# Performance work log

Hardware: AMD Instinct MI355X
Metric: run time of the kernel (lower is better)

Reference implementation:

```python
import jax, jax.numpy as jnp
import numpy as np

EMBED_DIM = 1024
VALUE_DIM = 2048
NUM_HEADS = 8
KEY_DIM = EMBED_DIM // NUM_HEADS      # 128
HEAD_DIM = VALUE_DIM // NUM_HEADS     # 256
B, T = 2, 2048
EPS = 1e-6


def _rotate_every_two(x):
    # x: [..., d] with d even; pairs (x0,x1)->(-x1,x0)
    x1 = x[..., ::2]
    x2 = x[..., 1::2]
    return jnp.stack((-x2, x1), axis=-1).reshape(x.shape)


def _theta_shift(x, sin, cos):
    # sin/cos: [T, key_dim] broadcast over [B, H, T, key_dim]
    return x * cos + _rotate_every_two(x) * sin


def setup_inputs() -> dict:
    key = jax.random.key(0)
    ks = jax.random.split(key, 6)
    x = jax.random.normal(ks[0], (B, T, EMBED_DIM), dtype=jnp.float32)

    # rotary angles as in torchscale RetNetRelPos
    angle = 1.0 / (10000.0 ** jnp.linspace(0.0, 1.0, KEY_DIM // 2))
    angle = jnp.repeat(angle, 2)                       # [key_dim], interleaved pairs
    idx = jnp.arange(T, dtype=jnp.float32)
    sin = jnp.sin(idx[:, None] * angle[None, :])       # [T, key_dim]
    cos = jnp.cos(idx[:, None] * angle[None, :])

    # per-head decay mask, normalized by sqrt(row-sum) as in RetNet
    decay = jnp.log(1.0 - 2.0 ** (-5.0 - jnp.arange(NUM_HEADS, dtype=jnp.float32)))
    diff = idx[:, None] - idx[None, :]                 # [T, T]
    exponent = jnp.where(diff >= 0, decay[:, None, None] * diff[None], -jnp.inf)
    mask = jnp.exp(exponent)                           # [H, T, T], lower-triangular decay
    mask = mask / jnp.sqrt(mask.sum(-1, keepdims=True))

    s = 0.02
    Wq = s * jax.random.normal(ks[1], (EMBED_DIM, EMBED_DIM), dtype=jnp.float32)
    Wk = s * jax.random.normal(ks[2], (EMBED_DIM, EMBED_DIM), dtype=jnp.float32)
    Wv = s * jax.random.normal(ks[3], (EMBED_DIM, VALUE_DIM), dtype=jnp.float32)
    Wg = s * jax.random.normal(ks[4], (EMBED_DIM, VALUE_DIM), dtype=jnp.float32)
    Wo = s * jax.random.normal(ks[5], (VALUE_DIM, EMBED_DIM), dtype=jnp.float32)
    return {"x": x, "sin": sin, "cos": cos, "mask": mask,
            "Wq": Wq, "Wk": Wk, "Wv": Wv, "Wg": Wg, "Wo": Wo}


def reference(x, sin, cos, mask, Wq, Wk, Wv, Wg, Wo):
    bsz, tgt_len, _ = x.shape
    scaling = KEY_DIM ** (-0.5)

    q = x @ Wq
    k = (x @ Wk) * scaling
    v = x @ Wv
    g = x @ Wg

    q = q.reshape(bsz, tgt_len, NUM_HEADS, KEY_DIM).transpose(0, 2, 1, 3)  # [B,H,T,kd]
    k = k.reshape(bsz, tgt_len, NUM_HEADS, KEY_DIM).transpose(0, 2, 1, 3)
    qr = _theta_shift(q, sin, cos)
    kr = _theta_shift(k, sin, cos)

    vr = v.reshape(bsz, tgt_len, NUM_HEADS, HEAD_DIM).transpose(0, 2, 1, 3)  # [B,H,T,hd]

    # parallel retention: decay-masked QK^T with abs-sum normalization (detached)
    qk = jnp.einsum('bhtd,bhsd->bhts', qr, kr) * mask[None]
    denom = jnp.clip(jnp.sum(jnp.abs(jax.lax.stop_gradient(qk)), axis=-1, keepdims=True),
                     1.0, 50000.0)
    qk = qk / denom
    out = jnp.einsum('bhts,bhsd->bhtd', qk, vr)          # [B,H,T,hd]
    out = out.transpose(0, 2, 1, 3)                      # [B,T,H,hd]

    # per-head RMSNorm (no affine)
    out = out * jax.lax.rsqrt(jnp.mean(out * out, axis=-1, keepdims=True) + EPS)
    out = out.reshape(bsz, tgt_len, VALUE_DIM)

    out = jax.nn.silu(g) * out
    return out @ Wo
```

## Files before the change

kernel.cpp:

```cpp
#include <hip/hip_runtime.h>
#include <hip/hip_bf16.h>
#include <math.h>

constexpr int T_SEQ = 2048;
constexpr int BB    = 2;
constexpr int EMBED = 1024;
constexpr int VDIM  = 2048;
constexpr int NHEADS = 8;
constexpr int KDIM  = 128;
constexpr int HDIM  = 256;
constexpr int ROWS  = BB * T_SEQ;
constexpr float EPS = 1e-6f;

typedef float  f32x4  __attribute__((ext_vector_type(4)));
typedef __bf16 bf16x8 __attribute__((ext_vector_type(8)));
typedef __bf16 bf16x4 __attribute__((ext_vector_type(4)));

__device__ __forceinline__ void gload16(const void* g, void* l) {
    __builtin_amdgcn_global_load_lds(
        (__attribute__((address_space(1))) void*)g,
        (__attribute__((address_space(3))) void*)l, 16, 0, 0);
}

#define WAITV(n) asm volatile("s_waitcnt vmcnt(" #n ")" ::: "memory")
#define BARRIER() __builtin_amdgcn_s_barrier()

__global__ __launch_bounds__(256)
void prep_all(const float* __restrict__ x, const float* __restrict__ Wq,
              const float* __restrict__ Wk, const float* __restrict__ Wv,
              const float* __restrict__ Wg, const float* __restrict__ Wo,
              __bf16* __restrict__ xb,
              __bf16* __restrict__ WqT, __bf16* __restrict__ WkT,
              __bf16* __restrict__ WvT, __bf16* __restrict__ WgT,
              __bf16* __restrict__ WoT) {
    const int bid = blockIdx.x;
    const int x_ = threadIdx.x, y_ = threadIdx.y;
    if (bid >= 8192) {
        const int i = (bid - 8192) * 256 + y_ * 32 + x_;
        float4 v = reinterpret_cast<const float4*>(x)[i];
        bf16x4 o = { (__bf16)v.x, (__bf16)v.y, (__bf16)v.z, (__bf16)v.w };
        reinterpret_cast<bf16x4*>(xb)[i] = o;
        return;
    }
    const float* W; __bf16* WT; int K, N, cx, cy;
    if (bid < 1024)      { W = Wq; WT = WqT; K = 1024; N = 1024; int rm = bid;        cx = rm & 31; cy = rm >> 5; }
    else if (bid < 2048) { W = Wk; WT = WkT; K = 1024; N = 1024; int rm = bid - 1024; cx = rm & 31; cy = rm >> 5; }
    else if (bid < 4096) { W = Wv; WT = WvT; K = 1024; N = 2048; int rm = bid - 2048; cx = rm & 63; cy = rm >> 6; }
    else if (bid < 6144) { W = Wg; WT = WgT; K = 1024; N = 2048; int rm = bid - 4096; cx = rm & 63; cy = rm >> 6; }
    else                 { W = Wo; WT = WoT; K = 2048; N = 1024; int rm = bid - 6144; cx = rm & 31; cy = rm >> 5; }

    __shared__ float tile[32][33];
    const int c0 = cx * 32, k0 = cy * 32;
    #pragma unroll
    for (int p = 0; p < 4; ++p)
        tile[y_ + p * 8][x_] = W[(size_t)(k0 + y_ + p * 8) * N + c0 + x_];
    __syncthreads();
    #pragma unroll
    for (int p = 0; p < 4; ++p)
        WT[(size_t)(c0 + y_ + p * 8) * K + k0 + x_] = (__bf16)tile[x_][y_ + p * 8];
}

__global__ __launch_bounds__(256)
void gemm_qk(const __bf16* __restrict__ A, const __bf16* __restrict__ BT,
             __bf16* __restrict__ Qb, __bf16* __restrict__ Kb,
             const float* __restrict__ sinT, const float* __restrict__ cosT) {
    constexpr int K = EMBED;
    __shared__ __align__(16) char smem[32768];
    __bf16* As = (__bf16*)smem;
    __bf16* Bs = (__bf16*)(smem + 16384);

    const int bid = blockIdx.x;
    const int rr = bid >> 3;
    const int bx = (bid & 7) * 2 + (rr & 1);
    const int by = rr >> 1;
    const int rowBase = by * 128;
    const int colBase = bx * 128;

    const int tid = threadIdx.x;
    const int w = tid >> 6, lane = tid & 63;
    const int g = lane >> 4, r = lane & 15;
    const int wm = w >> 1, wn = w & 1;

    const int vr  = lane >> 3;
    const int swz = ((lane & 7) ^ vr) * 8;
    const __bf16* aSb = A  + (size_t)(rowBase + 32 * w + vr) * K + swz;
    const __bf16* bSb = BT + (size_t)(colBase + 32 * w + vr) * K + swz;

    f32x4 acc[4][4];
    #pragma unroll
    for (int i = 0; i < 4; ++i)
        #pragma unroll
        for (int j = 0; j < 4; ++j)
            acc[i][j] = (f32x4){0.f, 0.f, 0.f, 0.f};

    for (int k0 = 0; k0 < K; k0 += 64) {
        __syncthreads();
        #pragma unroll
        for (int p = 0; p < 4; ++p) {
            const int cc = 4 * w + p;
            gload16(aSb + (size_t)(8 * p) * K + k0, smem         + cc * 1024);
            gload16(bSb + (size_t)(8 * p) * K + k0, smem + 16384 + cc * 1024);
        }
        __syncthreads();

        #pragma unroll
        for (int kk = 0; kk < 2; ++kk) {
            bf16x8 bfrag[4];
            #pragma unroll
            for (int nf = 0; nf < 4; ++nf) {
                const int row = wn * 64 + nf * 16 + r;
                bfrag[nf] = *reinterpret_cast<const bf16x8*>(
                    &Bs[row * 64 + (((kk << 2) + g) ^ (r & 7)) * 8]);
            }
            #pragma unroll
            for (int mf = 0; mf < 4; ++mf) {
                const int row = wm * 64 + mf * 16 + r;
                bf16x8 a = *reinterpret_cast<const bf16x8*>(
                    &As[row * 64 + (((kk << 2) + g) ^ (r & 7)) * 8]);
                #pragma unroll
                for (int nf = 0; nf < 4; ++nf)
                    acc[mf][nf] = __builtin_amdgcn_mfma_f32_16x16x32_bf16(a, bfrag[nf], acc[mf][nf], 0, 0, 0);
            }
        }
    }

    constexpr float kscale = 0.08838834764831845f;
    __bf16* dst; int cofs; float alphaSeg;
    if (colBase < 1024) { dst = Qb; cofs = colBase;        alphaSeg = 1.0f;   }
    else                { dst = Kb; cofs = colBase - 1024; alphaSeg = kscale; }

    #pragma unroll
    for (int mf = 0; mf < 4; ++mf)
        #pragma unroll
        for (int nf = 0; nf < 4; ++nf)
            #pragma unroll
            for (int j = 0; j < 4; ++j) {
                const int row  = rowBase + wm * 64 + mf * 16 + g * 4 + j;
                const int colL = cofs + wn * 64 + nf * 16 + r;
                float v = acc[mf][nf][j] * alphaSeg;
                const float p = __shfl_xor(v, 1);
                const int t  = row & (T_SEQ - 1);
                const int dh = colL & (KDIM - 1);
                const float c = cosT[t * KDIM + dh];
                const float s = sinT[t * KDIM + dh];
                v = (r & 1) ? (v * c + p * s) : (v * c - p * s);
                dst[(size_t)row * 1024 + colL] = (__bf16)v;
            }
}

#define STAGEH(ISB, TAU, HF) do { \
    const __bf16* s_ = ((ISB) ? BT : A) + \
        (size_t)((((ISB) ? colBase : rowBase)) + (HF) * 128 + w * 8 + srow) * 1024 + \
        (TAU) * 64 + swz; \
    char* d_ = smem + ((ISB) ? 65536 : 0) + (((TAU) & 1) * 2 + (HF)) * 16384 + w * 1024; \
    gload16(s_, d_); \
    gload16(s_ + (size_t)64 * 1024, d_ + 8192); \
} while (0)

#define QPHASE(TAU, Q, STGSTMT) do { \
    const int p_ = (TAU) & 1; \
    const __bf16* Ab_ = (const __bf16*)(smem + (p_ * 2 + wm) * 16384); \
    const __bf16* Bb_ = (const __bf16*)(smem + 65536 + (p_ * 2 + bh) * 16384); \
    if ((Q) == 0) { \
        _Pragma("unroll") for (int nf = 0; nf < 4; ++nf) \
        _Pragma("unroll") for (int kk = 0; kk < 2; ++kk) \
            bq[nf][kk] = *(const bf16x8*)(Bb_ + (bro + nf * 16) * 64 + ((kk * 4 + g) ^ rx) * 8); \
    } \
    bf16x8 aq_[2][2]; \
    _Pragma("unroll") for (int i = 0; i < 2; ++i) \
    _Pragma("unroll") for (int kk = 0; kk < 2; ++kk) \
        aq_[i][kk] = *(const bf16x8*)(Ab_ + (((Q) * 2 + i) * 16 + r) * 64 + ((kk * 4 + g) ^ rx) * 8); \
    STGSTMT; \
    BARRIER(); \
    __builtin_amdgcn_s_setprio(1); \
    _Pragma("unroll") for (int i = 0; i < 2; ++i) \
    _Pragma("unroll") for (int nf = 0; nf < 4; ++nf) \
    _Pragma("unroll") for (int kk = 0; kk < 2; ++kk) \
        acc[(Q) * 2 + i][nf] = __builtin_amdgcn_mfma_f32_16x16x32_bf16( \
            aq_[i][kk], bq[nf][kk], acc[(Q) * 2 + i][nf], 0, 0, 0); \
    __builtin_amdgcn_s_setprio(0); \
} while (0)

__global__ __launch_bounds__(512, 2)
void gemm_vg(const __bf16* __restrict__ A, const __bf16* __restrict__ BT,
             __bf16* __restrict__ Vt, __bf16* __restrict__ Gb) {
    __shared__ __align__(16) char smem[131072];

    const int bid = blockIdx.x;
    const int j2 = bid >> 3;
    const int bxA = (bid & 7) * 2 + (j2 & 1);
    const int by  = j2 >> 1;
    const int rowBase = by * 256;
    const int colBase = 2048 + bxA * 256;

    const int tid = threadIdx.x;
    const int w = tid >> 6, lane = tid & 63;
    const int g = lane >> 4, r = lane & 15;
    const int wm = w >> 2, wn = w & 3;
    const int rx = r & 7;
    const int bh = wn >> 1;
    const int bro = (wn & 1) * 64 + r;

    const int srow = lane >> 3;
    const int swz  = ((lane & 7) ^ srow) * 8;

    f32x4 acc[8][4];
    #pragma unroll
    for (int i = 0; i < 8; ++i)
        #pragma unroll
        for (int j = 0; j < 4; ++j)
            acc[i][j] = (f32x4){0.f, 0.f, 0.f, 0.f};
    bf16x8 bq[4][2];

    STAGEH(1, 0, 0); STAGEH(1, 0, 1);
    STAGEH(0, 0, 0); STAGEH(0, 0, 1);
    STAGEH(1, 1, 0); STAGEH(1, 1, 1);
    WAITV(4);
    BARRIER();

    for (int it = 0; it < 8; ++it) {
        const int e = 2 * it, o = e + 1;
        const bool more = (it < 7);
        QPHASE(e, 0, STAGEH(0, o, 0));                        BARRIER();
        QPHASE(e, 1, STAGEH(0, o, 1));                        BARRIER();
        QPHASE(e, 2, if (more) STAGEH(1, e + 2, 0));          BARRIER();
        QPHASE(e, 3, if (more) STAGEH(1, e + 2, 1));
        if (more) { WAITV(4); } else { WAITV(0); }            BARRIER();
        QPHASE(o, 0, if (more) STAGEH(0, e + 2, 0));          BARRIER();
        QPHASE(o, 1, if (more) STAGEH(0, e + 2, 1));          BARRIER();
        QPHASE(o, 2, if (more) STAGEH(1, o + 2, 0));          BARRIER();
        QPHASE(o, 3, if (more) STAGEH(1, o + 2, 1));
        if (more) { WAITV(4); } else { WAITV(0); }            BARRIER();
    }

    if (bxA < 8) {
        __bf16* Es = (__bf16*)smem + w * 4608;
        const int colV0 = (colBase - 2048) + wn * 64;
        const int h = colV0 >> 8, dd0 = colV0 & 255;
        const int li = lane & 7, rgrp = lane >> 3;
        #pragma unroll
        for (int h2 = 0; h2 < 2; ++h2) {
            #pragma unroll
            for (int mf = 0; mf < 4; ++mf)
                #pragma unroll
                for (int nf = 0; nf < 4; ++nf) {
                    f32x4 a = acc[h2 * 4 + mf][nf];
                    bf16x4 v = { (__bf16)a[0], (__bf16)a[1], (__bf16)a[2], (__bf16)a[3] };
                    *reinterpret_cast<bf16x4*>(&Es[(nf * 16 + r) * 72 + mf * 16 + g * 4]) = v;
                }
            __syncthreads();
            const int t0g = rowBase + wm * 128 + h2 * 64;
            const int bq_ = t0g >> 11, tl = t0g & 2047;
            __bf16* vtb = Vt + ((size_t)(bq_ * NHEADS + h) * HDIM + dd0) * T_SEQ + tl;
            #pragma unroll
            for (int c = 0; c < 8; ++c) {
                const int drow = 8 * c + rgrp;
                bf16x8 v = *reinterpret_cast<const bf16x8*>(&Es[drow * 72 + li * 8]);
                *reinterpret_cast<bf16x8*>(vtb + (size_t)drow * T_SEQ + li * 8) = v;
            }
            __syncthreads();
        }
        return;
    }

    const int cofs = colBase - 4096;
    #pragma unroll
    for (int mf = 0; mf < 8; ++mf)
        #pragma unroll
        for (int nf = 0; nf < 4; ++nf)
            #pragma unroll
            for (int j = 0; j < 4; ++j) {
                const int row  = rowBase + wm * 128 + mf * 16 + g * 4 + j;
                const int colL = cofs + wn * 64 + nf * 16 + r;
                Gb[(size_t)row * 2048 + colL] = (__bf16)acc[mf][nf][j];
            }
}

__global__ __launch_bounds__(256)
void gemm_wo(const __bf16* __restrict__ A, const __bf16* __restrict__ BT,
             float* __restrict__ C) {
    constexpr int N = EMBED, K = VDIM;
    __shared__ __align__(16) char smem[24576];
    __bf16* As = (__bf16*)smem;
    __bf16* Bs = (__bf16*)(smem + 8192);

    const int bid = blockIdx.x;
    const int swzb = (bid & 7) * 64 + (bid >> 3);
    const int rowBase = (swzb >> 3) * 64;
    const int colBase = (swzb & 7) * 128;

    const int tid = threadIdx.x;
    const int w = tid >> 6, lane = tid & 63;
    const int g = lane >> 4, r = lane & 15;
    const int wm = w >> 1, wn = w & 1;

    const int vr  = lane >> 3;
    const int swz = ((lane & 7) ^ vr) * 8;
    const __bf16* aSb = A  + (size_t)(rowBase + 16 * w + vr) * K + swz;
    const __bf16* bSb = BT + (size_t)(colBase + 32 * w + vr) * K + swz;

    f32x4 acc[2][4];
    #pragma unroll
    for (int i = 0; i < 2; ++i)
        #pragma unroll
        for (int j = 0; j < 4; ++j)
            acc[i][j] = (f32x4){0.f, 0.f, 0.f, 0.f};

    for (int k0 = 0; k0 < K; k0 += 64) {
        __syncthreads();
        #pragma unroll
        for (int p = 0; p < 2; ++p) {
            const int cc = 2 * w + p;
            gload16(aSb + (size_t)(8 * p) * K + k0, smem + cc * 1024);
        }
        #pragma unroll
        for (int p = 0; p < 4; ++p) {
            const int cc = 4 * w + p;
            gload16(bSb + (size_t)(8 * p) * K + k0, smem + 8192 + cc * 1024);
        }
        __syncthreads();

        #pragma unroll
        for (int kk = 0; kk < 2; ++kk) {
            bf16x8 bfrag[4];
            #pragma unroll
            for (int nf = 0; nf < 4; ++nf) {
                const int row = wn * 64 + nf * 16 + r;
                bfrag[nf] = *reinterpret_cast<const bf16x8*>(
                    &Bs[row * 64 + (((kk << 2) + g) ^ (r & 7)) * 8]);
            }
            #pragma unroll
            for (int mf = 0; mf < 2; ++mf) {
                const int row = wm * 32 + mf * 16 + r;
                bf16x8 a = *reinterpret_cast<const bf16x8*>(
                    &As[row * 64 + (((kk << 2) + g) ^ (r & 7)) * 8]);
                #pragma unroll
                for (int nf = 0; nf < 4; ++nf)
                    acc[mf][nf] = __builtin_amdgcn_mfma_f32_16x16x32_bf16(a, bfrag[nf], acc[mf][nf], 0, 0, 0);
            }
        }
    }

    #pragma unroll
    for (int mf = 0; mf < 2; ++mf)
        #pragma unroll
        for (int nf = 0; nf < 4; ++nf)
            #pragma unroll
            for (int j = 0; j < 4; ++j) {
                const int row = rowBase + wm * 32 + mf * 16 + g * 4 + j;
                const int col = colBase + wn * 64 + nf * 16 + r;
                C[(size_t)row * N + col] = acc[mf][nf][j];
            }
}

__global__ __launch_bounds__(256)
void retention_mfma(const __bf16* __restrict__ Qb, const __bf16* __restrict__ Kb,
                    const __bf16* __restrict__ Vt,
                    const __bf16* __restrict__ Gb, __bf16* __restrict__ Yb) {
    const int tid = threadIdx.x;
    const int w = tid >> 6, lane = tid & 63;
    const int g = lane >> 4, r = lane & 15;
    const int rx = r & 7;
    const int bid = blockIdx.x;
    const int h = bid & 7;
    const int slot = bid >> 3;
    const int b = slot & 1;
    const int x = slot >> 1;
    const int qt = (b == 0) ? (31 - x) : x;
    const int tt0 = qt * 64;
    const int trow0 = w * 16;

    __shared__ __align__(16) __bf16 Ks[2][64][128];
    __shared__ __align__(16) __bf16 Vs[256][64];
    __shared__ __align__(16) __bf16 Ps[4][16][72];

    const float rho   = 1.0f - exp2f(-(float)(5 + h));
    const float l2r   = log2f(rho);
    const float inv1m = exp2f((float)(5 + h));
    int   tj[4];
    float nrm[4];
    #pragma unroll
    for (int j = 0; j < 4; ++j) {
        tj[j] = tt0 + trow0 + g * 4 + j;
        nrm[j] = rsqrtf((1.0f - exp2f(l2r * (float)(tj[j] + 1))) * inv1m);
    }
    float pneg[4];
    #pragma unroll
    for (int ssub = 0; ssub < 4; ++ssub)
        pneg[ssub] = exp2f(-l2r * (float)(ssub * 16 + r));

    bf16x8 qf[4];
    {
        const __bf16* qrow = Qb + ((size_t)(b * T_SEQ + tt0 + trow0 + r)) * EMBED + h * KDIM;
        #pragma unroll
        for (int kb = 0; kb < 4; ++kb)
            qf[kb] = *reinterpret_cast<const bf16x8*>(qrow + kb * 32 + g * 8);
    }

    f32x4 acc[16];
    #pragma unroll
    for (int db = 0; db < 16; ++db) acc[db] = (f32x4){0.f, 0.f, 0.f, 0.f};
    float dsum[4] = {0.f, 0.f, 0.f, 0.f};

    const __bf16* vtbase = Vt + ((size_t)(b * NHEADS + h) * HDIM) * T_SEQ;
    const __bf16* kbase  = Kb + ((size_t)(b * T_SEQ)) * EMBED + h * KDIM;

    const int klr = lane >> 4;
    const int kc  = lane & 15;
    const int kswz_even = (kc ^ klr) * 8;
    const int kswz_odd  = (kc ^ (4 + klr)) * 8;
    const int vlr  = lane >> 3;
    const int vswz = ((lane & 7) ^ vlr) * 8;

    #pragma unroll
    for (int p = 0; p < 4; ++p) {
        const int cc = 4 * w + p;
        const int se = (p & 1) ? kswz_odd : kswz_even;
        gload16(kbase + (size_t)(4 * cc + klr) * EMBED + se,
                (char*)&Ks[0][0][0] + cc * 1024);
    }

    int cur = 0;
    const int nS = qt + 1;
    for (int st = 0; st < nS; ++st) {
        const int ss0 = st * 64;
        WAITV(0);
        BARRIER();

        #pragma unroll
        for (int p = 0; p < 8; ++p) {
            const int cc = 8 * w + p;
            gload16(vtbase + (size_t)(8 * cc + vlr) * T_SEQ + ss0 + vswz,
                    (char*)&Vs[0][0] + cc * 1024);
        }
        const bool more = (st + 1 < nS);
        if (more) {
            const int ssn = ss0 + 64;
            #pragma unroll
            for (int p = 0; p < 4; ++p) {
                const int cc = 4 * w + p;
                const int se = (p & 1) ? kswz_odd : kswz_even;
                gload16(kbase + (size_t)(ssn + 4 * cc + klr) * EMBED + se,
                        (char*)&Ks[cur ^ 1][0][0] + cc * 1024);
            }
        }

        float wj[4];
        #pragma unroll
        for (int j = 0; j < 4; ++j)
            wj[j] = exp2f(l2r * (float)(tj[j] - ss0)) * nrm[j];
        const bool diag = (st == qt);

        __builtin_amdgcn_s_setprio(1);
        #pragma unroll
        for (int ssub = 0; ssub < 4; ++ssub) {
            f32x4 sacc = (f32x4){0.f, 0.f, 0.f, 0.f};
            #pragma unroll
            for (int kb = 0; kb < 4; ++kb) {
                bf16x8 kf = *reinterpret_cast<const bf16x8*>(
                    &Ks[cur][ssub * 16 + r][((kb * 4 + g) ^ rx) * 8]);
                sacc = __builtin_amdgcn_mfma_f32_16x16x32_bf16(qf[kb], kf, sacc, 0, 0, 0);
            }
            const int scol = ss0 + ssub * 16 + r;
            const float mfac = pneg[ssub];
            #pragma unroll
            for (int j = 0; j < 4; ++j) {
                float pv = sacc[j] * (wj[j] * mfac);
                if (diag && scol > tj[j]) pv = 0.f;
                dsum[j] += fabsf(pv);
                Ps[w][g * 4 + j][ssub * 16 + r] = (__bf16)pv;
            }
        }
        __builtin_amdgcn_s_setprio(0);

        if (more) { WAITV(4); } else { WAITV(0); }
        BARRIER();

        __builtin_amdgcn_s_setprio(1);
        #pragma unroll
        for (int sh = 0; sh < 2; ++sh) {
            bf16x8 pf = *reinterpret_cast<const bf16x8*>(&Ps[w][r][sh * 32 + g * 8]);
            #pragma unroll
            for (int db = 0; db < 16; ++db) {
                bf16x8 vf = *reinterpret_cast<const bf16x8*>(
                    &Vs[db * 16 + r][((sh * 4 + g) ^ rx) * 8]);
                acc[db] = __builtin_amdgcn_mfma_f32_16x16x32_bf16(pf, vf, acc[db], 0, 0, 0);
            }
        }
        __builtin_amdgcn_s_setprio(0);
        cur ^= 1;
    }

    #pragma unroll
    for (int j = 0; j < 4; ++j) {
        float v = dsum[j];
        v += __shfl_xor(v, 1); v += __shfl_xor(v, 2);
        v += __shfl_xor(v, 4); v += __shfl_xor(v, 8);
        dsum[j] = fminf(fmaxf(v, 1.0f), 50000.0f);
    }
    float ss[4] = {0.f, 0.f, 0.f, 0.f};
    #pragma unroll
    for (int db = 0; db < 16; ++db)
        #pragma unroll
        for (int j = 0; j < 4; ++j) {
            const float v = acc[db][j] / dsum[j];
            acc[db][j] = v;
            ss[j] = fmaf(v, v, ss[j]);
        }
    #pragma unroll
    for (int j = 0; j < 4; ++j) {
        float v = ss[j];
        v += __shfl_xor(v, 1); v += __shfl_xor(v, 2);
        v += __shfl_xor(v, 4); v += __shfl_xor(v, 8);
        ss[j] = rsqrtf(v * (1.0f / 256.0f) + EPS);
    }
    #pragma unroll
    for (int j = 0; j < 4; ++j) {
        const size_t row = (size_t)(b * T_SEQ + tj[j]);
        const __bf16* grow = Gb + row * VDIM + h * HDIM;
        __bf16* yrow = Yb + row * VDIM + h * HDIM;
        #pragma unroll
        for (int db = 0; db < 16; ++db) {
            const int c = db * 16 + r;
            const float gv = (float)grow[c];
            const float sil = gv / (1.0f + expf(-gv));
            yrow[c] = (__bf16)(sil * acc[db][j] * ss[j]);
        }
    }
}

extern "C" void kernel_launch(void* const* d_in, const int* in_sizes, int n_in,
                              void* d_out, int out_size, void* d_ws, size_t ws_size,
                              hipStream_t stream) {
    (void)in_sizes; (void)n_in; (void)out_size; (void)ws_size;

    const float* x    = (const float*)d_in[0];
    const float* sinT = (const float*)d_in[1];
    const float* cosT = (const float*)d_in[2];
    const float* Wq   = (const float*)d_in[4];
    const float* Wk   = (const float*)d_in[5];
    const float* Wv   = (const float*)d_in[6];
    const float* Wg   = (const float*)d_in[7];
    const float* Wo   = (const float*)d_in[8];
    float* out = (float*)d_out;

    char* wsp = (char*)d_ws;
    __bf16* xb  = (__bf16*)(wsp);
    __bf16* WqT = (__bf16*)(wsp + (8u  << 20));
    __bf16* WkT = (__bf16*)(wsp + (10u << 20));
    __bf16* WvT = (__bf16*)(wsp + (12u << 20));
    __bf16* WgT = (__bf16*)(wsp + (16u << 20));
    __bf16* WoT = (__bf16*)(wsp + (20u << 20));
    __bf16* Qb  = (__bf16*)(wsp + (24u << 20));
    __bf16* Kb  = (__bf16*)(wsp + (32u << 20));
    __bf16* Yb  = (__bf16*)(wsp + (40u << 20));
    __bf16* Gb  = (__bf16*)(wsp + (56u << 20));
    __bf16* Vt  = (__bf16*)(wsp + (72u << 20));
    __bf16* WTall = WqT;

    const dim3 blk(256);
    const dim3 tblk(32, 8);

    prep_all<<<12288, tblk, 0, stream>>>(x, Wq, Wk, Wv, Wg, Wo,
                                         xb, WqT, WkT, WvT, WgT, WoT);

    gemm_qk<<<512, blk, 0, stream>>>(xb, WTall, Qb, Kb, sinT, cosT);

    gemm_vg<<<256, 512, 0, stream>>>(xb, WTall, Vt, Gb);

    retention_mfma<<<512, blk, 0, stream>>>(Qb, Kb, Vt, Gb, Yb);

    gemm_wo<<<512, blk, 0, stream>>>(Yb, WoT, out);
}
```

Baseline: 172.1 us.

## Split PV matmul by value columns across waves with shared P tile

The P·V stage now has each wave compute all 64 query rows for its own 64-column slice of the value dimension. Before, each wave handled its 16 rows across all 256 columns. P is written into a shared 64x72 tile, so each V fragment read from LDS feeds four MFMAs instead of one, cutting LDS traffic for V. In exchange, P reads go up, the P tile now needs an lgkmcnt wait before the barrier, and the row normalizer and RMS sums must be exchanged through shared memory with two extra block syncs in the epilogue.

```diff
diff --git a/kernel.cpp b/kernel.cpp
--- a/kernel.cpp
+++ b/kernel.cpp
@@ -23,6 +23,7 @@
 }
 
 #define WAITV(n) asm volatile("s_waitcnt vmcnt(" #n ")" ::: "memory")
+#define WAITLGKM() asm volatile("s_waitcnt lgkmcnt(0)" ::: "memory")
 #define BARRIER() __builtin_amdgcn_s_barrier()
 
 __global__ __launch_bounds__(256)
@@ -372,7 +373,9 @@
 
     __shared__ __align__(16) __bf16 Ks[2][64][128];
     __shared__ __align__(16) __bf16 Vs[256][64];
-    __shared__ __align__(16) __bf16 Ps[4][16][72];
+    __shared__ __align__(16) __bf16 Ps[64][72];
+    __shared__ float dsumL[64];
+    __shared__ float ssL[4][64];
 
     const float rho   = 1.0f - exp2f(-(float)(5 + h));
     const float l2r   = log2f(rho);
@@ -397,9 +400,12 @@
             qf[kb] = *reinterpret_cast<const bf16x8*>(qrow + kb * 32 + g * 8);
     }
 
-    f32x4 acc[16];
-    #pragma unroll
-    for (int db = 0; db < 16; ++db) acc[db] = (f32x4){0.f, 0.f, 0.f, 0.f};
+    f32x4 acc[4][4];
+    #pragma unroll
+    for (int qs = 0; qs < 4; ++qs)
+        #pragma unroll
+        for (int ds = 0; ds < 4; ++ds)
+            acc[qs][ds] = (f32x4){0.f, 0.f, 0.f, 0.f};
     float dsum[4] = {0.f, 0.f, 0.f, 0.f};
 
     const __bf16* vtbase = Vt + ((size_t)(b * NHEADS + h) * HDIM) * T_SEQ;
@@ -468,23 +474,30 @@
                 float pv = sacc[j] * (wj[j] * mfac);
                 if (diag && scol > tj[j]) pv = 0.f;
                 dsum[j] += fabsf(pv);
-                Ps[w][g * 4 + j][ssub * 16 + r] = (__bf16)pv;
+                Ps[trow0 + g * 4 + j][ssub * 16 + r] = (__bf16)pv;
             }
         }
         __builtin_amdgcn_s_setprio(0);
 
         if (more) { WAITV(4); } else { WAITV(0); }
+        WAITLGKM();
         BARRIER();
 
         __builtin_amdgcn_s_setprio(1);
         #pragma unroll
         for (int sh = 0; sh < 2; ++sh) {
-            bf16x8 pf = *reinterpret_cast<const bf16x8*>(&Ps[w][r][sh * 32 + g * 8]);
-            #pragma unroll
-            for (int db = 0; db < 16; ++db) {
+            bf16x8 pf[4];
+            #pragma unroll
+            for (int qs = 0; qs < 4; ++qs)
+                pf[qs] = *reinterpret_cast<const bf16x8*>(
+                    &Ps[qs * 16 + r][sh * 32 + g * 8]);
+            #pragma unroll
+            for (int ds = 0; ds < 4; ++ds) {
                 bf16x8 vf = *reinterpret_cast<const bf16x8*>(
-                    &Vs[db * 16 + r][((sh * 4 + g) ^ rx) * 8]);
-                acc[db] = __builtin_amdgcn_mfma_f32_16x16x32_bf16(pf, vf, acc[db], 0, 0, 0);
+                    &Vs[w * 64 + ds * 16 + r][((sh * 4 + g) ^ rx) * 8]);
+                #pragma unroll
+                for (int qs = 0; qs < 4; ++qs)
+                    acc[qs][ds] = __builtin_amdgcn_mfma_f32_16x16x32_bf16(pf[qs], vf, acc[qs][ds], 0, 0, 0);
             }
         }
         __builtin_amdgcn_s_setprio(0);
@@ -498,35 +511,49 @@
         v += __shfl_xor(v, 4); v += __shfl_xor(v, 8);
         dsum[j] = fminf(fmaxf(v, 1.0f), 50000.0f);
     }
-    float ss[4] = {0.f, 0.f, 0.f, 0.f};
-    #pragma unroll
-    for (int db = 0; db < 16; ++db)
+    if (r == 0) {
+        #pragma unroll
+        for (int j = 0; j < 4; ++j)
+            dsumL[trow0 + g * 4 + j] = dsum[j];
+    }
+    __syncthreads();
+
+    #pragma unroll
+    for (int qs = 0; qs < 4; ++qs)
         #pragma unroll
         for (int j = 0; j < 4; ++j) {
-            const float v = acc[db][j] / dsum[j];
-            acc[db][j] = v;
-            ss[j] = fmaf(v, v, ss[j]);
-        }
-    #pragma unroll
-    for (int j = 0; j < 4; ++j) {
-        float v = ss[j];
-        v += __shfl_xor(v, 1); v += __shfl_xor(v, 2);
-        v += __shfl_xor(v, 4); v += __shfl_xor(v, 8);
-        ss[j] = rsqrtf(v * (1.0f / 256.0f) + EPS);
-    }
-    #pragma unroll
-    for (int j = 0; j < 4; ++j) {
-        const size_t row = (size_t)(b * T_SEQ + tj[j]);
-        const __bf16* grow = Gb + row * VDIM + h * HDIM;
-        __bf16* yrow = Yb + row * VDIM + h * HDIM;
-        #pragma unroll
-        for (int db = 0; db < 16; ++db) {
-            const int c = db * 16 + r;
-            const float gv = (float)grow[c];
-            const float sil = gv / (1.0f + expf(-gv));
-            yrow[c] = (__bf16)(sil * acc[db][j] * ss[j]);
-        }
-    }
+            const float inv = 1.0f / dsumL[qs * 16 + g * 4 + j];
+            float sp = 0.f;
+            #pragma unroll
+            for (int ds = 0; ds < 4; ++ds) {
+                const float v = acc[qs][ds][j] * inv;
+                acc[qs][ds][j] = v;
+                sp = fmaf(v, v, sp);
+            }
+            sp += __shfl_xor(sp, 1); sp += __shfl_xor(sp, 2);
+            sp += __shfl_xor(sp, 4); sp += __shfl_xor(sp, 8);
+            if (r == 0) ssL[w][qs * 16 + g * 4 + j] = sp;
+        }
+    __syncthreads();
+
+    #pragma unroll
+    for (int qs = 0; qs < 4; ++qs)
+        #pragma unroll
+        for (int j = 0; j < 4; ++j) {
+            const int ql = qs * 16 + g * 4 + j;
+            const float tot = ssL[0][ql] + ssL[1][ql] + ssL[2][ql] + ssL[3][ql];
+            const float rs = rsqrtf(tot * (1.0f / 256.0f) + EPS);
+            const size_t row = (size_t)(b * T_SEQ + tt0 + ql);
+            const __bf16* grow = Gb + row * VDIM + h * HDIM;
+            __bf16* yrow = Yb + row * VDIM + h * HDIM;
+            #pragma unroll
+            for (int ds = 0; ds < 4; ++ds) {
+                const int c = w * 64 + ds * 16 + r;
+                const float gv = (float)grow[c];
+                const float sil = gv / (1.0f + expf(-gv));
+                yrow[c] = (__bf16)(sil * acc[qs][ds][j] * rs);
+            }
+        }
 }
 
 extern "C" void kernel_launch(void* const* d_in, const int* in_sizes, int n_in,
```

Result: no change. 171.2 us (-0.6%).
